# Performance work log

Measured on AMD Instinct MI355X. Metric: run time of the kernel, lower is better.

Reference implementation:

```python
import jax, jax.numpy as jnp
import numpy as np

NUM_LEVELS = 16
COARSEST = 16
FINEST = 1024
TABLE_SIZE = 524288  # max_hash_table_entries per level
FEAT = 2             # hash_table_feature_dim
DENSITY_W = 64
COLOR_W = 64
N_POINTS = 262144

PRIMES = jnp.array([1, 2654435761, 805459861], dtype=jnp.uint32)
# 8 cube corners: 1 -> ceil coordinate, 0 -> floor coordinate (matches source vertex_0..vertex_7)
CORNER_SEL = np.array([[1,1,1],[1,1,0],[1,0,1],[0,1,1],[1,0,0],[0,1,0],[0,0,1],[0,0,0]], dtype=bool)


def hash_encode(position, hash_table):
    # position: (N,3) in [0,1); hash_table: (NUM_LEVELS*TABLE_SIZE, FEAT)
    levels = jnp.arange(NUM_LEVELS)
    growth = jnp.exp((jnp.log(float(FINEST)) - jnp.log(float(COARSEST))) / (NUM_LEVELS - 1))
    scalings = jnp.floor(COARSEST * growth ** levels)            # (L,)
    scaled = position[:, None, :] * scalings[None, :, None]       # (N,L,3)
    floor = jnp.floor(scaled)
    ceil = jnp.ceil(scaled)
    sel = jnp.asarray(CORNER_SEL)[None, None]                     # (1,1,8,3)
    corners = jnp.where(sel, ceil[:, :, None, :], floor[:, :, None, :]).astype(jnp.uint32)  # (N,L,8,3)
    h = corners * PRIMES                                          # uint32 wrap-around mul
    idx = jnp.bitwise_xor(jnp.bitwise_xor(h[..., 0], h[..., 1]), h[..., 2]) % TABLE_SIZE
    idx = idx + (levels[None, :, None] * TABLE_SIZE).astype(jnp.uint32)  # (N,L,8)
    feats = hash_table[idx]                                       # (N,L,8,F) gather
    frac = scaled - floor                                         # (N,L,3)
    w = jnp.prod(jnp.where(sel, frac[:, :, None, :], 1.0 - frac[:, :, None, :]), axis=-1)  # (N,L,8)
    out = jnp.sum(feats * w[..., None], axis=2)                   # trilinear interp -> (N,L,F)
    return out.reshape(out.shape[0], NUM_LEVELS * FEAT)           # (N,32)


def sh_encode(d):
    # fourth-order spherical harmonics, vectorized over (N,3)
    x, y, z = d[:, 0], d[:, 1], d[:, 2]
    xx, yy, zz = x * x, y * y, z * z
    comps = [
        0.28209479177387814 * jnp.ones_like(x),
        0.4886025119029199 * y,
        0.4886025119029199 * z,
        0.4886025119029199 * x,
        1.0925484305920792 * x * y,
        1.0925484305920792 * y * z,
        0.9461746957575601 * zz - 0.31539156525252,
        1.0925484305920792 * x * z,
        0.5462742152960396 * (xx - yy),
        0.5900435899266435 * y * (3 * xx - yy),
        2.890611442640554 * x * y * z,
        0.4570457994644658 * y * (5 * zz - 1),
        0.3731763325901154 * z * (5 * zz - 3),
        0.4570457994644658 * x * (5 * zz - 1),
        1.445305721320277 * z * (xx - yy),
        0.5900435899266435 * x * (xx - 3 * yy),
    ]
    return jnp.stack(comps, axis=-1)  # (N,16)


def setup_inputs() -> dict:
    key = jax.random.key(0)
    ks = jax.random.split(key, 16)
    N = N_POINTS
    position = jax.random.uniform(ks[0], (N, 3), dtype=jnp.float32)
    direction = jax.random.normal(ks[1], (N, 3), dtype=jnp.float32)
    hash_table = jax.random.normal(ks[2], (NUM_LEVELS * TABLE_SIZE, FEAT), dtype=jnp.float32) * 1e-2
    enc_dim = NUM_LEVELS * FEAT  # 32
    def dense(k, fi, fo):
        return jax.random.normal(k, (fi, fo), dtype=jnp.float32) * (1.0 / np.sqrt(fi))
    return {
        "position": position,
        "direction": direction,
        "hash_table": hash_table,
        "w_d1": dense(ks[3], enc_dim, DENSITY_W), "b_d1": jnp.zeros((DENSITY_W,), jnp.float32),
        "w_d2": dense(ks[4], DENSITY_W, 16),      "b_d2": jnp.zeros((16,), jnp.float32),
        "w_c1": dense(ks[5], 16 + 16, COLOR_W),   "b_c1": jnp.zeros((COLOR_W,), jnp.float32),
        "w_c2": dense(ks[6], COLOR_W, COLOR_W),   "b_c2": jnp.zeros((COLOR_W,), jnp.float32),
        "w_c3": dense(ks[7], COLOR_W, 3),         "b_c3": jnp.zeros((3,), jnp.float32),
    }


def reference(position, direction, hash_table, w_d1, b_d1, w_d2, b_d2,
              w_c1, b_c1, w_c2, b_c2, w_c3, b_c3):
    enc_pos = hash_encode(position, hash_table)               # (N,32)
    h = jax.nn.relu(enc_pos @ w_d1 + b_d1)                    # (N,64)
    density = h @ w_d2 + b_d2                                 # (N,16)
    enc_dir = sh_encode(direction)                            # (N,16)
    x = jnp.concatenate([density, enc_dir], axis=-1)          # (N,32)
    x = jax.nn.relu(x @ w_c1 + b_c1)
    x = jax.nn.relu(x @ w_c2 + b_c2)
    x = x @ w_c3 + b_c3                                       # (N,3)
    color = jax.nn.sigmoid(x)                                 # high_dynamic_range=False
    return (density, color)
```

## Files before the change

### kernel.cpp

```cpp
#include <hip/hip_runtime.h>
#include <stdint.h>

#define NPTS 262144
#define TBL 524288u
#define TBL_MASK 524287u
#define NBINS 32768

#define WS_TAB_OFF   0u
#define WS_TAB_BYTES (16u * 524288u * 4u)
#define WS_ENC_OFF   WS_TAB_BYTES
#define WS_ENC_BYTES (16u * (uint32_t)NPTS * 4u)
#define WS_W_OFF     (WS_ENC_OFF + WS_ENC_BYTES)
#define WS_W_U32     4736
#define WS_HIST_OFF  (WS_W_OFF + WS_W_U32 * 4u)
#define WS_KEY_OFF   (WS_HIST_OFF + NBINS * 4u)
#define WS_IDX_OFF   (WS_KEY_OFF + (uint32_t)NPTS * 4u)
#define WS_PS_OFF    (WS_IDX_OFF + (uint32_t)NPTS * 4u)
#define WS_NEED_SORT ((size_t)WS_PS_OFF + (size_t)NPTS * 12u)
#define WS_NEED      ((size_t)WS_HIST_OFF)

#define PW_D1 0
#define PW_D2 1024
#define PW_C1 1536
#define PW_C2 2560
#define PW_C3 4608

typedef __attribute__((ext_vector_type(8))) _Float16 half8;
typedef __attribute__((ext_vector_type(4))) float f32x4;

__device__ const float d_scale[16] = {16.f, 21.f, 27.f, 36.f, 48.f, 64.f, 84.f, 111.f,
                                      147.f, 194.f, 256.f, 337.f, 445.f, 588.f, 776.f, 1024.f};

__device__ __forceinline__ uint16_t f2h(float f) {
    _Float16 h = (_Float16)f;
    return __builtin_bit_cast(uint16_t, h);
}
__device__ __forceinline__ uint32_t pack2(float lo, float hi) {
    return (uint32_t)f2h(lo) | ((uint32_t)f2h(hi) << 16);
}
__device__ __forceinline__ float h2f_lo(uint32_t v) {
    return (float)__builtin_bit_cast(_Float16, (uint16_t)(v & 0xffffu));
}
__device__ __forceinline__ float h2f_hi(uint32_t v) {
    return (float)__builtin_bit_cast(_Float16, (uint16_t)(v >> 16));
}

__device__ __forceinline__ half8 bfrag_p(const uint32_t* __restrict__ Wp, int N, int kofs, int nofs, int l) {
    const int kp0 = (kofs + ((l >> 4) << 3)) >> 1;
    const uint32_t* p = Wp + (size_t)kp0 * N + (nofs + (l & 15));
    union { uint32_t u[4]; half8 s; } r;
    r.u[0] = p[0 * N];
    r.u[1] = p[1 * N];
    r.u[2] = p[2 * N];
    r.u[3] = p[3 * N];
    return r.s;
}
__device__ __forceinline__ half8 bfrag3_p(const uint32_t* __restrict__ Wp, int kofs, int l) {
    const int kp0 = (kofs + ((l >> 4) << 3)) >> 1;
    const int n = l & 15;
    union { uint32_t u[4]; half8 s; } r;
    if (n < 3) {
        const uint32_t* p = Wp + (size_t)kp0 * 4 + n;
        r.u[0] = p[0]; r.u[1] = p[4]; r.u[2] = p[8]; r.u[3] = p[12];
    } else {
        r.u[0] = 0; r.u[1] = 0; r.u[2] = 0; r.u[3] = 0;
    }
    return r.s;
}

__device__ __forceinline__ half8 ld_a_h(const unsigned char* hcb, int mt, int kb, int l) {
    const int row = mt * 16 + (l & 15);
    uint32_t byte = (uint32_t)row * 128 + (uint32_t)kb * 64 + (uint32_t)((l >> 4) << 4);
    byte ^= (uint32_t)(row & 7) << 4;
    return *(const half8*)(hcb + byte);
}
__device__ __forceinline__ void st_h(unsigned char* hcb, int row, int col, float v) {
    uint32_t byte = (uint32_t)row * 128 + (uint32_t)col * 2;
    byte ^= (uint32_t)(row & 7) << 4;
    *(uint16_t*)(hcb + byte) = f2h(fmaxf(v, 0.f));
}

#define MFMA(a, b, c) __builtin_amdgcn_mfma_f32_16x16x32_f16((a), (b), (c), 0, 0, 0)

__global__ void __launch_bounds__(256) convert_tab(
    const float4* __restrict__ t, uint4* __restrict__ o, int n4,
    const float* __restrict__ wd1, const float* __restrict__ wd2,
    const float* __restrict__ wc1, const float* __restrict__ wc2,
    const float* __restrict__ wc3, uint32_t* __restrict__ wp)
{
    const int i = blockIdx.x * 256 + threadIdx.x;
    if (i < n4) {
        const float4 a = t[2 * i];
        const float4 b = t[2 * i + 1];
        o[i] = make_uint4(pack2(a.x, a.y), pack2(a.z, a.w),
                          pack2(b.x, b.y), pack2(b.z, b.w));
    }
    if (blockIdx.x == 0) {
        const int tid = threadIdx.x;
        for (int j = tid; j < 1024; j += 256) {
            const int kp = j >> 6, n = j & 63;
            wp[PW_D1 + j] = pack2(wd1[(2 * kp) * 64 + n], wd1[(2 * kp + 1) * 64 + n]);
        }
        for (int j = tid; j < 512; j += 256) {
            const int kp = j >> 4, n = j & 15;
            wp[PW_D2 + j] = pack2(wd2[(2 * kp) * 16 + n], wd2[(2 * kp + 1) * 16 + n]);
        }
        for (int j = tid; j < 1024; j += 256) {
            const int kp = j >> 6, n = j & 63;
            wp[PW_C1 + j] = pack2(wc1[(2 * kp) * 64 + n], wc1[(2 * kp + 1) * 64 + n]);
        }
        for (int j = tid; j < 2048; j += 256) {
            const int kp = j >> 6, n = j & 63;
            wp[PW_C2 + j] = pack2(wc2[(2 * kp) * 64 + n], wc2[(2 * kp + 1) * 64 + n]);
        }
        for (int j = tid; j < 128; j += 256) {
            const int kp = j >> 2, n = j & 3;
            wp[PW_C3 + j] = (n < 3) ? pack2(wc3[(2 * kp) * 3 + n], wc3[(2 * kp + 1) * 3 + n]) : 0u;
        }
    }
}

__device__ __forceinline__ uint32_t spread3(uint32_t x) {
    x &= 0x3FFu;
    x = (x | (x << 16)) & 0x030000FFu;
    x = (x | (x << 8))  & 0x0300F00Fu;
    x = (x | (x << 4))  & 0x030C30C3u;
    x = (x | (x << 2))  & 0x09249249u;
    return x;
}

__global__ void __launch_bounds__(256) kzero(uint32_t* __restrict__ hist) {
    hist[blockIdx.x * 256 + threadIdx.x] = 0u;
}

__global__ void __launch_bounds__(256) khist(
    const float* __restrict__ g_pos, uint32_t* __restrict__ key, uint32_t* __restrict__ hist)
{
    const int p = blockIdx.x * 256 + threadIdx.x;
    const float px = g_pos[3 * p + 0];
    const float py = g_pos[3 * p + 1];
    const float pz = g_pos[3 * p + 2];
    const uint32_t cx = min(31u, (uint32_t)(px * 32.f));
    const uint32_t cy = min(31u, (uint32_t)(py * 32.f));
    const uint32_t cz = min(31u, (uint32_t)(pz * 32.f));
    const uint32_t k = spread3(cx) | (spread3(cy) << 1) | (spread3(cz) << 2);
    key[p] = k;
    atomicAdd(&hist[k], 1u);
}

__global__ void __launch_bounds__(1024) kscan(uint32_t* __restrict__ hist) {
    const int tid = threadIdx.x;
    const int lane = tid & 63, wid = tid >> 6;
    __shared__ uint32_t wsum[16];
    __shared__ uint32_t carry;
    if (tid == 0) carry = 0;
    __syncthreads();
    for (int it = 0; it < NBINS / 1024; ++it) {
        const uint32_t v = hist[it * 1024 + tid];
        uint32_t s = v;
        #pragma unroll
        for (int d = 1; d < 64; d <<= 1) {
            const uint32_t t = __shfl_up(s, d);
            if (lane >= d) s += t;
        }
        if (lane == 63) wsum[wid] = s;
        __syncthreads();
        uint32_t woff = 0;
        for (int w = 0; w < wid; ++w) woff += wsum[w];
        const uint32_t excl = carry + woff + (s - v);
        hist[it * 1024 + tid] = excl;
        __syncthreads();
        if (tid == 1023) carry = excl + v;
        __syncthreads();
    }
}

__global__ void __launch_bounds__(256) kscatter(
    const float* __restrict__ g_pos, const uint32_t* __restrict__ key,
    uint32_t* __restrict__ hist, uint32_t* __restrict__ out_idx,
    float* __restrict__ pos_sorted)
{
    const int p = blockIdx.x * 256 + threadIdx.x;
    const uint32_t slot = atomicAdd(&hist[key[p]], 1u);
    out_idx[slot] = (uint32_t)p;
    pos_sorted[3 * slot + 0] = g_pos[3 * p + 0];
    pos_sorted[3 * slot + 1] = g_pos[3 * p + 1];
    pos_sorted[3 * slot + 2] = g_pos[3 * p + 2];
}

__global__ void __launch_bounds__(256) gather_enc2(
    const float* __restrict__ pos,
    const uint32_t* __restrict__ tab16,
    uint32_t* __restrict__ enc)
{
    const int b = blockIdx.x;
    const int x8 = b & 7;
    const int lev = (b >> 12) ? (15 - x8) : x8;
    const int pbase = (((b >> 3) & 511) << 9) + threadIdx.x;

    const float s = d_scale[lev];
    const uint32_t* t = tab16 + (size_t)lev * TBL;

    float tx[2], ty[2], tz[2];
    uint32_t idx0[2][4], idx1[2][4];
    bool odd[2];
    #pragma unroll
    for (int q = 0; q < 2; ++q) {
        const int p = pbase + q * 256;
        const float px = pos[3 * p + 0];
        const float py = pos[3 * p + 1];
        const float pz = pos[3 * p + 2];
        const float sx = px * s, sy = py * s, sz = pz * s;
        const float fx = floorf(sx), fy = floorf(sy), fz = floorf(sz);
        tx[q] = sx - fx; ty[q] = sy - fy; tz[q] = sz - fz;
        const uint32_t x0 = (uint32_t)fx, x1 = (uint32_t)ceilf(sx);
        const uint32_t hy0 = (uint32_t)fy * 2654435761u, hy1 = (uint32_t)ceilf(sy) * 2654435761u;
        const uint32_t hz0 = (uint32_t)fz * 805459861u,  hz1 = (uint32_t)ceilf(sz) * 805459861u;
        odd[q] = (x0 & 1u) != 0u;
        #pragma unroll
        for (int cp = 0; cp < 4; ++cp) {
            const uint32_t hyz = ((cp & 1) ? hy1 : hy0) ^ ((cp & 2) ? hz1 : hz0);
            idx0[q][cp] = (x0 ^ hyz) & TBL_MASK;
            idx1[q][cp] = (x1 ^ hyz) & TBL_MASK;
        }
    }
    uint2 v2[2][4];
    #pragma unroll
    for (int q = 0; q < 2; ++q)
        #pragma unroll
        for (int cp = 0; cp < 4; ++cp)
            v2[q][cp] = *reinterpret_cast<const uint2*>(t + (idx0[q][cp] & ~1u));
    uint32_t fup[2][4];
    #pragma unroll
    for (int q = 0; q < 2; ++q)
        #pragma unroll
        for (int cp = 0; cp < 4; ++cp)
            fup[q][cp] = odd[q] ? t[idx1[q][cp]] : 0u;
    #pragma unroll
    for (int q = 0; q < 2; ++q) {
        float e0 = 0.f, e1 = 0.f;
        #pragma unroll
        for (int cp = 0; cp < 4; ++cp) {
            const bool lo = (idx0[q][cp] & 1u) == 0u;
            const uint32_t v0 = lo ? v2[q][cp].x : v2[q][cp].y;
            uint32_t v1 = lo ? v2[q][cp].y : v2[q][cp].x;
            if (odd[q]) v1 = fup[q][cp];
            const float wyz = ((cp & 1) ? ty[q] : 1.f - ty[q]) * ((cp & 2) ? tz[q] : 1.f - tz[q]);
            const float w0 = (1.f - tx[q]) * wyz;
            const float w1 = tx[q] * wyz;
            e0 = fmaf(h2f_lo(v0), w0, fmaf(h2f_lo(v1), w1, e0));
            e1 = fmaf(h2f_hi(v0), w0, fmaf(h2f_hi(v1), w1, e1));
        }
        enc[(size_t)lev * NPTS + pbase + q * 256] = pack2(e0, e1);
    }
}

__global__ void __launch_bounds__(256, 3) nerf_mlp(
    const float* __restrict__ g_dir,
    const uint32_t* __restrict__ enc,
    const uint32_t* __restrict__ wp,
    const uint32_t* __restrict__ out_idx,
    const int use_perm,
    const float* __restrict__ g_bd1,
    const float* __restrict__ g_bd2,
    const float* __restrict__ g_bc1,
    const float* __restrict__ g_bc2,
    const float* __restrict__ g_bc3,
    float* __restrict__ g_out)
{
    __shared__ __align__(16) unsigned char s_lds[4 * 12288];
    unsigned char* wbase = s_lds + (threadIdx.x >> 6) * 12288;
    unsigned char* hcb  = wbase;
    unsigned char* xinb = wbase + 8192;

    const int l = threadIdx.x & 63;
    const int m_my = l >> 4;
    const int r_my = l & 15;
    const int wpt  = blockIdx.x * 256 + (threadIdx.x & 192);
    const int p    = wpt + l;

    #pragma unroll
    for (int kb = 0; kb < 4; ++kb) {
        uint4 w4;
        w4.x = enc[(size_t)(4 * kb + 0) * NPTS + p];
        w4.y = enc[(size_t)(4 * kb + 1) * NPTS + p];
        w4.z = enc[(size_t)(4 * kb + 2) * NPTS + p];
        w4.w = enc[(size_t)(4 * kb + 3) * NPTS + p];
        *(uint4*)(hcb + m_my * 1024 + (kb * 16 + r_my) * 16) = w4;
    }

    const uint32_t dp = use_perm ? out_idx[p] : (uint32_t)p;
    const float dx = g_dir[3 * dp + 0];
    const float dy = g_dir[3 * dp + 1];
    const float dz = g_dir[3 * dp + 2];

    {
        const float xx = dx * dx, yy = dy * dy, zz = dz * dz;
        float s[16];
        s[0]  = 0.28209479177387814f;
        s[1]  = 0.4886025119029199f * dy;
        s[2]  = 0.4886025119029199f * dz;
        s[3]  = 0.4886025119029199f * dx;
        s[4]  = 1.0925484305920792f * dx * dy;
        s[5]  = 1.0925484305920792f * dy * dz;
        s[6]  = 0.9461746957575601f * zz - 0.31539156525252f;
        s[7]  = 1.0925484305920792f * dx * dz;
        s[8]  = 0.5462742152960396f * (xx - yy);
        s[9]  = 0.5900435899266435f * dy * (3.f * xx - yy);
        s[10] = 2.890611442640554f * dx * dy * dz;
        s[11] = 0.4570457994644658f * dy * (5.f * zz - 1.f);
        s[12] = 0.3731763325901154f * dz * (5.f * zz - 3.f);
        s[13] = 0.4570457994644658f * dx * (5.f * zz - 1.f);
        s[14] = 1.445305721320277f * dz * (xx - yy);
        s[15] = 0.5900435899266435f * dx * (xx - 3.f * yy);
        *(uint4*)(xinb + m_my * 1024 + (32 + r_my) * 16) =
            make_uint4(pack2(s[0], s[1]), pack2(s[2], s[3]), pack2(s[4], s[5]), pack2(s[6], s[7]));
        *(uint4*)(xinb + m_my * 1024 + (48 + r_my) * 16) =
            make_uint4(pack2(s[8], s[9]), pack2(s[10], s[11]), pack2(s[12], s[13]), pack2(s[14], s[15]));
    }

    const int cl = l & 15;
    const int rg = (l >> 4) << 2;

    {
        f32x4 acc[4][4];
        half8 B[4];
        #pragma unroll
        for (int nt = 0; nt < 4; ++nt) {
            B[nt] = bfrag_p(wp + PW_D1, 64, 0, nt * 16, l);
            const float b = g_bd1[nt * 16 + cl];
            #pragma unroll
            for (int mt = 0; mt < 4; ++mt) acc[mt][nt] = (f32x4){b, b, b, b};
        }
        #pragma unroll
        for (int mt = 0; mt < 4; ++mt) {
            const half8 A = *(const half8*)(hcb + mt * 1024 + l * 16);
            #pragma unroll
            for (int nt = 0; nt < 4; ++nt) acc[mt][nt] = MFMA(A, B[nt], acc[mt][nt]);
        }
        #pragma unroll
        for (int mt = 0; mt < 4; ++mt)
            #pragma unroll
            for (int nt = 0; nt < 4; ++nt)
                #pragma unroll
                for (int r = 0; r < 4; ++r)
                    st_h(hcb, mt * 16 + rg + r, nt * 16 + cl, acc[mt][nt][r]);
    }

    {
        const half8 B0 = bfrag_p(wp + PW_D2, 16, 0,  0, l);
        const half8 B1 = bfrag_p(wp + PW_D2, 16, 32, 0, l);
        const float b = g_bd2[cl];
        #pragma unroll
        for (int mt = 0; mt < 4; ++mt) {
            f32x4 acc = (f32x4){b, b, b, b};
            acc = MFMA(ld_a_h(hcb, mt, 0, l), B0, acc);
            acc = MFMA(ld_a_h(hcb, mt, 1, l), B1, acc);
            #pragma unroll
            for (int r = 0; r < 4; ++r) {
                const int pt = wpt + mt * 16 + rg + r;
                const uint32_t opt = use_perm ? out_idx[pt] : (uint32_t)pt;
                g_out[(size_t)opt * 16 + cl] = acc[r];
                const uint32_t byte = (uint32_t)mt * 1024
                                    + (uint32_t)(((cl >> 3) * 16 + rg + r) * 16) + (uint32_t)(cl & 7) * 2;
                *(uint16_t*)(xinb + byte) = f2h(acc[r]);
            }
        }
    }

    {
        f32x4 acc[4][4];
        half8 B[4];
        #pragma unroll
        for (int nt = 0; nt < 4; ++nt) {
            B[nt] = bfrag_p(wp + PW_C1, 64, 0, nt * 16, l);
            const float b = g_bc1[nt * 16 + cl];
            #pragma unroll
            for (int mt = 0; mt < 4; ++mt) acc[mt][nt] = (f32x4){b, b, b, b};
        }
        #pragma unroll
        for (int mt = 0; mt < 4; ++mt) {
            const half8 A = *(const half8*)(xinb + mt * 1024 + l * 16);
            #pragma unroll
            for (int nt = 0; nt < 4; ++nt) acc[mt][nt] = MFMA(A, B[nt], acc[mt][nt]);
        }
        #pragma unroll
        for (int mt = 0; mt < 4; ++mt)
            #pragma unroll
            for (int nt = 0; nt < 4; ++nt)
                #pragma unroll
                for (int r = 0; r < 4; ++r)
                    st_h(hcb, mt * 16 + rg + r, nt * 16 + cl, acc[mt][nt][r]);
    }

    {
        f32x4 acc[4][4];
        #pragma unroll
        for (int nt = 0; nt < 4; ++nt) {
            const float b = g_bc2[nt * 16 + cl];
            #pragma unroll
            for (int mt = 0; mt < 4; ++mt) acc[mt][nt] = (f32x4){b, b, b, b};
        }
        #pragma unroll
        for (int kb = 0; kb < 2; ++kb) {
            half8 A[4];
            #pragma unroll
            for (int mt = 0; mt < 4; ++mt) A[mt] = ld_a_h(hcb, mt, kb, l);
            #pragma unroll
            for (int nt = 0; nt < 4; ++nt) {
                const half8 B = bfrag_p(wp + PW_C2, 64, kb * 32, nt * 16, l);
                #pragma unroll
                for (int mt = 0; mt < 4; ++mt) acc[mt][nt] = MFMA(A[mt], B, acc[mt][nt]);
            }
        }
        #pragma unroll
        for (int mt = 0; mt < 4; ++mt)
            #pragma unroll
            for (int nt = 0; nt < 4; ++nt)
                #pragma unroll
                for (int r = 0; r < 4; ++r)
                    st_h(hcb, mt * 16 + rg + r, nt * 16 + cl, acc[mt][nt][r]);
    }

    {
        const half8 B0 = bfrag3_p(wp + PW_C3, 0, l);
        const half8 B1 = bfrag3_p(wp + PW_C3, 32, l);
        const float b = (cl < 3) ? g_bc3[cl] : 0.f;
        #pragma unroll
        for (int mt = 0; mt < 4; ++mt) {
            f32x4 acc = (f32x4){b, b, b, b};
            acc = MFMA(ld_a_h(hcb, mt, 0, l), B0, acc);
            acc = MFMA(ld_a_h(hcb, mt, 1, l), B1, acc);
            if (cl < 3) {
                #pragma unroll
                for (int r = 0; r < 4; ++r) {
                    const int pt = wpt + mt * 16 + rg + r;
                    const uint32_t opt = use_perm ? out_idx[pt] : (uint32_t)pt;
                    g_out[(size_t)NPTS * 16 + (size_t)opt * 3 + cl] = 1.f / (1.f + expf(-acc[r]));
                }
            }
        }
    }
}

extern "C" void kernel_launch(void* const* d_in, const int* in_sizes, int n_in,
                              void* d_out, int out_size, void* d_ws, size_t ws_size,
                              hipStream_t stream) {
    uint32_t* tab16 = (uint32_t*)((char*)d_ws + WS_TAB_OFF);
    uint32_t* enc   = (uint32_t*)((char*)d_ws + WS_ENC_OFF);
    uint32_t* wpk   = (uint32_t*)((char*)d_ws + WS_W_OFF);
    uint32_t* hist  = (uint32_t*)((char*)d_ws + WS_HIST_OFF);
    uint32_t* key   = (uint32_t*)((char*)d_ws + WS_KEY_OFF);
    uint32_t* oidx  = (uint32_t*)((char*)d_ws + WS_IDX_OFF);
    float*    psort = (float*)((char*)d_ws + WS_PS_OFF);

    const float* g_pos = (const float*)d_in[0];
    const float* g_dir = (const float*)d_in[1];

    convert_tab<<<8192, 256, 0, stream>>>(
        (const float4*)d_in[2], (uint4*)tab16, 2097152,
        (const float*)d_in[3], (const float*)d_in[5],
        (const float*)d_in[7], (const float*)d_in[9],
        (const float*)d_in[11], wpk);

    if (ws_size >= WS_NEED_SORT) {
        kzero<<<NBINS / 256, 256, 0, stream>>>(hist);
        khist<<<NPTS / 256, 256, 0, stream>>>(g_pos, key, hist);
        kscan<<<1, 1024, 0, stream>>>(hist);
        kscatter<<<NPTS / 256, 256, 0, stream>>>(g_pos, key, hist, oidx, psort);
        gather_enc2<<<8192, 256, 0, stream>>>(psort, tab16, enc);
        nerf_mlp<<<NPTS / 256, 256, 0, stream>>>(
            g_dir, enc, wpk, oidx, 1,
            (const float*)d_in[4], (const float*)d_in[6],
            (const float*)d_in[8], (const float*)d_in[10],
            (const float*)d_in[12],
            (float*)d_out);
    } else {
        gather_enc2<<<8192, 256, 0, stream>>>(g_pos, tab16, enc);
        nerf_mlp<<<NPTS / 256, 256, 0, stream>>>(
            g_dir, enc, wpk, nullptr, 0,
            (const float*)d_in[4], (const float*)d_in[6],
            (const float*)d_in[8], (const float*)d_in[10],
            (const float*)d_in[12],
            (float*)d_out);
    }
}
```

Measured before the change: 185.9 us.

## Fuse table conversion with histogram, rewrite scan, pre-sort directions in scatter

Merges the hash-table fp16 conversion kernel and the Morton histogram kernel into one launch, with blocks partitioned by index. The single-block prefix scan now handles 32 bins per thread in registers with one barrier instead of looping 32 times with several barriers each. The scatter pass also writes directions in sorted order, so the MLP reads them contiguously instead of through the permutation. This saves launches and random direction loads at the cost of an extra sorted buffer and one more write pass.

```diff
diff --git a/kernel.cpp b/kernel.cpp
--- a/kernel.cpp
+++ b/kernel.cpp
@@ -16,7 +16,8 @@
 #define WS_KEY_OFF   (WS_HIST_OFF + NBINS * 4u)
 #define WS_IDX_OFF   (WS_KEY_OFF + (uint32_t)NPTS * 4u)
 #define WS_PS_OFF    (WS_IDX_OFF + (uint32_t)NPTS * 4u)
-#define WS_NEED_SORT ((size_t)WS_PS_OFF + (size_t)NPTS * 12u)
+#define WS_DS_OFF    (WS_PS_OFF + (uint32_t)NPTS * 12u)
+#define WS_NEED_SORT ((size_t)WS_DS_OFF + (size_t)NPTS * 12u)
 #define WS_NEED      ((size_t)WS_HIST_OFF)
 
 #define PW_D1 0
@@ -82,44 +83,6 @@
 
 #define MFMA(a, b, c) __builtin_amdgcn_mfma_f32_16x16x32_f16((a), (b), (c), 0, 0, 0)
 
-__global__ void __launch_bounds__(256) convert_tab(
-    const float4* __restrict__ t, uint4* __restrict__ o, int n4,
-    const float* __restrict__ wd1, const float* __restrict__ wd2,
-    const float* __restrict__ wc1, const float* __restrict__ wc2,
-    const float* __restrict__ wc3, uint32_t* __restrict__ wp)
-{
-    const int i = blockIdx.x * 256 + threadIdx.x;
-    if (i < n4) {
-        const float4 a = t[2 * i];
-        const float4 b = t[2 * i + 1];
-        o[i] = make_uint4(pack2(a.x, a.y), pack2(a.z, a.w),
-                          pack2(b.x, b.y), pack2(b.z, b.w));
-    }
-    if (blockIdx.x == 0) {
-        const int tid = threadIdx.x;
-        for (int j = tid; j < 1024; j += 256) {
-            const int kp = j >> 6, n = j & 63;
-            wp[PW_D1 + j] = pack2(wd1[(2 * kp) * 64 + n], wd1[(2 * kp + 1) * 64 + n]);
-        }
-        for (int j = tid; j < 512; j += 256) {
-            const int kp = j >> 4, n = j & 15;
-            wp[PW_D2 + j] = pack2(wd2[(2 * kp) * 16 + n], wd2[(2 * kp + 1) * 16 + n]);
-        }
-        for (int j = tid; j < 1024; j += 256) {
-            const int kp = j >> 6, n = j & 63;
-            wp[PW_C1 + j] = pack2(wc1[(2 * kp) * 64 + n], wc1[(2 * kp + 1) * 64 + n]);
-        }
-        for (int j = tid; j < 2048; j += 256) {
-            const int kp = j >> 6, n = j & 63;
-            wp[PW_C2 + j] = pack2(wc2[(2 * kp) * 64 + n], wc2[(2 * kp + 1) * 64 + n]);
-        }
-        for (int j = tid; j < 128; j += 256) {
-            const int kp = j >> 2, n = j & 3;
-            wp[PW_C3 + j] = (n < 3) ? pack2(wc3[(2 * kp) * 3 + n], wc3[(2 * kp + 1) * 3 + n]) : 0u;
-        }
-    }
-}
-
 __device__ __forceinline__ uint32_t spread3(uint32_t x) {
     x &= 0x3FFu;
     x = (x | (x << 16)) & 0x030000FFu;
@@ -133,52 +96,99 @@
     hist[blockIdx.x * 256 + threadIdx.x] = 0u;
 }
 
-__global__ void __launch_bounds__(256) khist(
-    const float* __restrict__ g_pos, uint32_t* __restrict__ key, uint32_t* __restrict__ hist)
+__global__ void __launch_bounds__(256) convert_hist(
+    const float4* __restrict__ t, uint4* __restrict__ o,
+    const float* __restrict__ wd1, const float* __restrict__ wd2,
+    const float* __restrict__ wc1, const float* __restrict__ wc2,
+    const float* __restrict__ wc3, uint32_t* __restrict__ wp,
+    const float* __restrict__ g_pos, uint32_t* __restrict__ key,
+    uint32_t* __restrict__ hist)
 {
-    const int p = blockIdx.x * 256 + threadIdx.x;
-    const float px = g_pos[3 * p + 0];
-    const float py = g_pos[3 * p + 1];
-    const float pz = g_pos[3 * p + 2];
-    const uint32_t cx = min(31u, (uint32_t)(px * 32.f));
-    const uint32_t cy = min(31u, (uint32_t)(py * 32.f));
-    const uint32_t cz = min(31u, (uint32_t)(pz * 32.f));
-    const uint32_t k = spread3(cx) | (spread3(cy) << 1) | (spread3(cz) << 2);
-    key[p] = k;
-    atomicAdd(&hist[k], 1u);
+    const int blk = blockIdx.x;
+    if (blk < 8192) {
+        const int i = blk * 256 + threadIdx.x;
+        const float4 a = t[2 * i];
+        const float4 b = t[2 * i + 1];
+        o[i] = make_uint4(pack2(a.x, a.y), pack2(a.z, a.w),
+                          pack2(b.x, b.y), pack2(b.z, b.w));
+        if (blk == 0) {
+            const int tid = threadIdx.x;
+            for (int j = tid; j < 1024; j += 256) {
+                const int kp = j >> 6, n = j & 63;
+                wp[PW_D1 + j] = pack2(wd1[(2 * kp) * 64 + n], wd1[(2 * kp + 1) * 64 + n]);
+            }
+            for (int j = tid; j < 512; j += 256) {
+                const int kp = j >> 4, n = j & 15;
+                wp[PW_D2 + j] = pack2(wd2[(2 * kp) * 16 + n], wd2[(2 * kp + 1) * 16 + n]);
+            }
+            for (int j = tid; j < 1024; j += 256) {
+                const int kp = j >> 6, n = j & 63;
+                wp[PW_C1 + j] = pack2(wc1[(2 * kp) * 64 + n], wc1[(2 * kp + 1) * 64 + n]);
+            }
+            for (int j = tid; j < 2048; j += 256) {
+                const int kp = j >> 6, n = j & 63;
+                wp[PW_C2 + j] = pack2(wc2[(2 * kp) * 64 + n], wc2[(2 * kp + 1) * 64 + n]);
+            }
+            for (int j = tid; j < 128; j += 256) {
+                const int kp = j >> 2, n = j & 3;
+                wp[PW_C3 + j] = (n < 3) ? pack2(wc3[(2 * kp) * 3 + n], wc3[(2 * kp + 1) * 3 + n]) : 0u;
+            }
+        }
+    } else {
+        const int p = (blk - 8192) * 256 + threadIdx.x;
+        const float px = g_pos[3 * p + 0];
+        const float py = g_pos[3 * p + 1];
+        const float pz = g_pos[3 * p + 2];
+        const uint32_t cx = min(31u, (uint32_t)(px * 32.f));
+        const uint32_t cy = min(31u, (uint32_t)(py * 32.f));
+        const uint32_t cz = min(31u, (uint32_t)(pz * 32.f));
+        const uint32_t k = spread3(cx) | (spread3(cy) << 1) | (spread3(cz) << 2);
+        key[p] = k;
+        atomicAdd(&hist[k], 1u);
+    }
 }
 
 __global__ void __launch_bounds__(1024) kscan(uint32_t* __restrict__ hist) {
     const int tid = threadIdx.x;
     const int lane = tid & 63, wid = tid >> 6;
-    __shared__ uint32_t wsum[16];
-    __shared__ uint32_t carry;
-    if (tid == 0) carry = 0;
+    uint4* hp = (uint4*)(hist + tid * 32);
+    uint4 a[8];
+    #pragma unroll
+    for (int i = 0; i < 8; ++i) a[i] = hp[i];
+    uint32_t S = 0;
+    #pragma unroll
+    for (int i = 0; i < 8; ++i) S += a[i].x + a[i].y + a[i].z + a[i].w;
+
+    uint32_t s = S;
+    #pragma unroll
+    for (int d = 1; d < 64; d <<= 1) {
+        const uint32_t t = __shfl_up(s, d);
+        if (lane >= d) s += t;
+    }
+    __shared__ uint32_t ws[16];
+    if (lane == 63) ws[wid] = s;
     __syncthreads();
-    for (int it = 0; it < NBINS / 1024; ++it) {
-        const uint32_t v = hist[it * 1024 + tid];
-        uint32_t s = v;
-        #pragma unroll
-        for (int d = 1; d < 64; d <<= 1) {
-            const uint32_t t = __shfl_up(s, d);
-            if (lane >= d) s += t;
-        }
-        if (lane == 63) wsum[wid] = s;
-        __syncthreads();
-        uint32_t woff = 0;
-        for (int w = 0; w < wid; ++w) woff += wsum[w];
-        const uint32_t excl = carry + woff + (s - v);
-        hist[it * 1024 + tid] = excl;
-        __syncthreads();
-        if (tid == 1023) carry = excl + v;
-        __syncthreads();
+    uint32_t woff = 0;
+    for (int w = 0; w < wid; ++w) woff += ws[w];
+    uint32_t run = woff + (s - S);
+
+    #pragma unroll
+    for (int i = 0; i < 8; ++i) {
+        uint4 v = a[i];
+        uint4 o;
+        o.x = run; run += v.x;
+        o.y = run; run += v.y;
+        o.z = run; run += v.z;
+        o.w = run; run += v.w;
+        hp[i] = o;
     }
 }
 
 __global__ void __launch_bounds__(256) kscatter(
-    const float* __restrict__ g_pos, const uint32_t* __restrict__ key,
+    const float* __restrict__ g_pos, const float* __restrict__ g_dir,
+    const uint32_t* __restrict__ key,
     uint32_t* __restrict__ hist, uint32_t* __restrict__ out_idx,
-    float* __restrict__ pos_sorted)
+    float* __restrict__ pos_sorted, float* __restrict__ dir_sorted)
 {
     const int p = blockIdx.x * 256 + threadIdx.x;
     const uint32_t slot = atomicAdd(&hist[key[p]], 1u);
@@ -186,6 +196,9 @@
     pos_sorted[3 * slot + 0] = g_pos[3 * p + 0];
     pos_sorted[3 * slot + 1] = g_pos[3 * p + 1];
     pos_sorted[3 * slot + 2] = g_pos[3 * p + 2];
+    dir_sorted[3 * slot + 0] = g_dir[3 * p + 0];
+    dir_sorted[3 * slot + 1] = g_dir[3 * p + 1];
+    dir_sorted[3 * slot + 2] = g_dir[3 * p + 2];
 }
 
 __global__ void __launch_bounds__(256) gather_enc2(
@@ -289,10 +302,9 @@
         *(uint4*)(hcb + m_my * 1024 + (kb * 16 + r_my) * 16) = w4;
     }
 
-    const uint32_t dp = use_perm ? out_idx[p] : (uint32_t)p;
-    const float dx = g_dir[3 * dp + 0];
-    const float dy = g_dir[3 * dp + 1];
-    const float dz = g_dir[3 * dp + 2];
+    const float dx = g_dir[3 * p + 0];
+    const float dy = g_dir[3 * p + 1];
+    const float dz = g_dir[3 * p + 2];
 
     {
         const float xx = dx * dx, yy = dy * dy, zz = dz * dz;
@@ -453,29 +465,35 @@
     uint32_t* key   = (uint32_t*)((char*)d_ws + WS_KEY_OFF);
     uint32_t* oidx  = (uint32_t*)((char*)d_ws + WS_IDX_OFF);
     float*    psort = (float*)((char*)d_ws + WS_PS_OFF);
+    float*    dsort = (float*)((char*)d_ws + WS_DS_OFF);
 
     const float* g_pos = (const float*)d_in[0];
     const float* g_dir = (const float*)d_in[1];
 
-    convert_tab<<<8192, 256, 0, stream>>>(
-        (const float4*)d_in[2], (uint4*)tab16, 2097152,
-        (const float*)d_in[3], (const float*)d_in[5],
-        (const float*)d_in[7], (const float*)d_in[9],
-        (const float*)d_in[11], wpk);
-
     if (ws_size >= WS_NEED_SORT) {
         kzero<<<NBINS / 256, 256, 0, stream>>>(hist);
-        khist<<<NPTS / 256, 256, 0, stream>>>(g_pos, key, hist);
+        convert_hist<<<9216, 256, 0, stream>>>(
+            (const float4*)d_in[2], (uint4*)tab16,
+            (const float*)d_in[3], (const float*)d_in[5],
+            (const float*)d_in[7], (const float*)d_in[9],
+            (const float*)d_in[11], wpk,
+            g_pos, key, hist);
         kscan<<<1, 1024, 0, stream>>>(hist);
-        kscatter<<<NPTS / 256, 256, 0, stream>>>(g_pos, key, hist, oidx, psort);
+        kscatter<<<NPTS / 256, 256, 0, stream>>>(g_pos, g_dir, key, hist, oidx, psort, dsort);
         gather_enc2<<<8192, 256, 0, stream>>>(psort, tab16, enc);
         nerf_mlp<<<NPTS / 256, 256, 0, stream>>>(
-            g_dir, enc, wpk, oidx, 1,
+            dsort, enc, wpk, oidx, 1,
             (const float*)d_in[4], (const float*)d_in[6],
             (const float*)d_in[8], (const float*)d_in[10],
             (const float*)d_in[12],
             (float*)d_out);
     } else {
+        convert_hist<<<8192, 256, 0, stream>>>(
+            (const float4*)d_in[2], (uint4*)tab16,
+            (const float*)d_in[3], (const float*)d_in[5],
+            (const float*)d_in[7], (const float*)d_in[9],
+            (const float*)d_in[11], wpk,
+            g_pos, nullptr, nullptr);
         gather_enc2<<<8192, 256, 0, stream>>>(g_pos, tab16, enc);
         nerf_mlp<<<NPTS / 256, 256, 0, stream>>>(
             g_dir, enc, wpk, nullptr, 0,
```

Result: faster. 162.8 us (-12.4%).
